# Optimization experiments

Hardware: AMD Instinct MI355X
Metric: run time of the kernel (lower is better)

## Reference

```python
import jax, jax.numpy as jnp
import numpy as np

DIM = 256
N = 8192

def setup_inputs() -> dict:
    key = jax.random.key(0)
    kx, kq, kk, kv = jax.random.split(key, 4)
    X = jax.random.normal(kx, (N, DIM), dtype=jnp.float32)
    # nn.Linear weights are [out, in]; xavier-uniform-like scale via normal/sqrt(dim)
    Wq = jax.random.normal(kq, (DIM, DIM), dtype=jnp.float32) / np.sqrt(DIM)
    Wk = jax.random.normal(kk, (DIM, DIM), dtype=jnp.float32) / np.sqrt(DIM)
    Wv = jax.random.normal(kv, (DIM, DIM), dtype=jnp.float32) / np.sqrt(DIM)
    return {"X": X, "Wq": Wq, "Wk": Wk, "Wv": Wv}

def reference(X, Wq, Wk, Wv):
    # nn.Linear(no bias): y = X @ W.T
    Q = X @ Wq.T  # [N, D]
    K = X @ Wk.T
    V = X @ Wv.T
    scores = (Q @ K.T) / jnp.sqrt(jnp.asarray(DIM, dtype=X.dtype))  # [N, N]
    softed = jax.nn.softmax(scores, axis=-1)
    return softed @ V  # [N, D]
```

## Files before the change

### kernel.cpp

```cpp
#include <hip/hip_runtime.h>
#include <math.h>

#define N 8192
#define D 256
#define QBLK 128
#define KBLK 32

typedef float f32x4 __attribute__((ext_vector_type(4)));
typedef float f32x16 __attribute__((ext_vector_type(16)));
typedef short bf16x8 __attribute__((ext_vector_type(8)));

#define MFMA16(a, b, c) __builtin_amdgcn_mfma_f32_16x16x32_bf16((a), (b), (c), 0, 0, 0)
#define MFMA32(a, b, c) __builtin_amdgcn_mfma_f32_32x32x16_bf16((a), (b), (c), 0, 0, 0)
#define BAR() __builtin_amdgcn_s_barrier()
#define CFENCE() asm volatile("" ::: "memory")

__device__ __forceinline__ unsigned short f2b(float f) {
    unsigned u = __builtin_bit_cast(unsigned, f);
    u = u + 0x7fffu + ((u >> 16) & 1u);
    return (unsigned short)(u >> 16);
}
__device__ __forceinline__ unsigned pk2(float a, float b) {
    return (unsigned)f2b(a) | ((unsigned)f2b(b) << 16);
}
__device__ __forceinline__ unsigned cvtpk(float a, float b) {
    unsigned r;
    asm("v_cvt_pk_bf16_f32 %0, %1, %2" : "=v"(r) : "v"(a), "v"(b));
    return r;
}
__device__ __forceinline__ float b2f(short s) {
    unsigned x = ((unsigned)(unsigned short)s) << 16;
    return __builtin_bit_cast(float, x);
}

__global__ __launch_bounds__(256) void proj_mfma(
    const float* __restrict__ X, const float* __restrict__ Wq,
    const float* __restrict__ Wk, const float* __restrict__ Wv,
    unsigned short* __restrict__ Qb, unsigned short* __restrict__ Kb,
    unsigned short* __restrict__ Vt)
{
    __shared__ char Wl[32768];
    const int z = blockIdx.z;
    const float* W = (z == 0) ? Wq : (z == 1) ? Wk : Wv;
    const int r0 = blockIdx.x * 64;
    const int c0 = blockIdx.y * 64;
    const int t = threadIdx.x, w = t >> 6, l = t & 63;
    const int lo = l & 15, hi = l >> 4;

    #pragma unroll
    for (int i = 0; i < 16; ++i) {
        int e4 = t + i * 256;
        int col = e4 >> 6, kk4 = e4 & 63;
        float4 f = *(const float4*)&W[(size_t)(c0 + col) * D + kk4 * 4];
        unsigned long long v = (unsigned long long)pk2(f.x, f.y)
                             | ((unsigned long long)pk2(f.z, f.w) << 32);
        *(unsigned long long*)(Wl + col * 512 + ((kk4 * 8) ^ ((col & 7) << 4))) = v;
    }
    __syncthreads();

    bf16x8 xf[8];
    {
        const float* xr = X + (size_t)(r0 + w * 16 + lo) * D;
        #pragma unroll
        for (int ks = 0; ks < 8; ++ks) {
            float4 a = *(const float4*)(xr + ks * 32 + hi * 8);
            float4 b = *(const float4*)(xr + ks * 32 + hi * 8 + 4);
            bf16x8 v;
            v[0] = (short)f2b(a.x); v[1] = (short)f2b(a.y);
            v[2] = (short)f2b(a.z); v[3] = (short)f2b(a.w);
            v[4] = (short)f2b(b.x); v[5] = (short)f2b(b.y);
            v[6] = (short)f2b(b.z); v[7] = (short)f2b(b.w);
            xf[ks] = v;
        }
    }

    f32x4 acc[4];
    #pragma unroll
    for (int nc = 0; nc < 4; ++nc) acc[nc] = (f32x4){0.f, 0.f, 0.f, 0.f};
    #pragma unroll
    for (int ks = 0; ks < 8; ++ks) {
        #pragma unroll
        for (int nc = 0; nc < 4; ++nc) {
            int col = nc * 16 + lo;
            bf16x8 wf = *(const bf16x8*)(Wl + col * 512 +
                                         ((ks * 64 + hi * 16) ^ ((col & 7) << 4)));
            acc[nc] = MFMA16(xf[ks], wf, acc[nc]);
        }
    }

    if (z < 2) {
        unsigned short* Y = z ? Kb : Qb;
        #pragma unroll
        for (int nc = 0; nc < 4; ++nc)
            #pragma unroll
            for (int r = 0; r < 4; ++r)
                Y[(size_t)(r0 + w * 16 + hi * 4 + r) * D + c0 + nc * 16 + lo] = f2b(acc[nc][r]);
    } else {
        #pragma unroll
        for (int nc = 0; nc < 4; ++nc) {
            unsigned long long v = (unsigned long long)pk2(acc[nc][0], acc[nc][1])
                                 | ((unsigned long long)pk2(acc[nc][2], acc[nc][3]) << 32);
            *(unsigned long long*)&Vt[(size_t)(c0 + nc * 16 + lo) * N + r0 + w * 16 + hi * 4] = v;
        }
    }
}

template <int KSPLIT>
__global__ __launch_bounds__(256, 2) void attn_mfma(
    const unsigned short* __restrict__ Qb,
    const unsigned short* __restrict__ Kb,
    const unsigned short* __restrict__ Vt,
    unsigned short* __restrict__ Opart,
    float2* __restrict__ ml)
{
    extern __shared__ char smem[];
    const int t = threadIdx.x;
    const int w = t >> 6;
    const int l = t & 63;
    const int r = l & 31;
    const int hi1 = l >> 5;
    const int bid = blockIdx.x;
    const int split = bid % KSPLIT;
    const int xblk = bid / KSPLIT;
    const int q0 = xblk * QBLK + w * 32;
    const int kbase = split * (N / KSPLIT);
    const int NTS = N / KSPLIT / KBLK;
    const int p0 = bid & (NTS - 1);

    unsigned ksoff[4], vsoff[4];
    #pragma unroll
    for (int i = 0; i < 4; ++i) {
        int c = t + i * 256;
        int rr = c >> 5, xc = c & 31;
        int pk = (rr & 0x13) | ((rr & 4) << 1) | ((rr & 8) >> 1);
        ksoff[i] = (unsigned)(pk * D + (xc ^ (rr & 7)) * 8);
        int dd = c >> 2, x2 = c & 3;
        vsoff[i] = (unsigned)(dd * N + (x2 ^ ((dd >> 1) & 3)) * 8);
    }

    auto stageK = [&](char* kbuf, int tile) {
        const unsigned koff = (unsigned)(kbase + tile * KBLK) * D;
        #pragma unroll
        for (int i = 0; i < 4; ++i)
            __builtin_amdgcn_global_load_lds(
                (const __attribute__((address_space(1))) void*)(Kb + koff + ksoff[i]),
                (__attribute__((address_space(3))) void*)(kbuf + (t + i * 256) * 16), 16, 0, 0);
    };
    auto stageV = [&](char* vbuf, int tile) {
        const unsigned voff = (unsigned)(kbase + tile * KBLK);
        #pragma unroll
        for (int i = 0; i < 4; ++i)
            __builtin_amdgcn_global_load_lds(
                (const __attribute__((address_space(1))) void*)(Vt + voff + vsoff[i]),
                (__attribute__((address_space(3))) void*)(vbuf + (t + i * 256) * 16), 16, 0, 0);
    };

    bf16x8 qf[16];
    {
        const unsigned short* qrow = Qb + (size_t)(q0 + r) * D;
        #pragma unroll
        for (int ks = 0; ks < 16; ++ks)
            qf[ks] = *(const bf16x8*)(qrow + ks * 16 + hi1 * 8);
    }

    stageK(smem, p0);
    stageV(smem + 32768, p0);
    stageK(smem + 16384, (p0 + 1) & (NTS - 1));
    stageV(smem + 32768 + 16384, (p0 + 1) & (NTS - 1));

    f32x16 Oacc[8];
    #pragma unroll
    for (int nc = 0; nc < 8; ++nc)
        #pragma unroll
        for (int e = 0; e < 16; ++e) Oacc[nc][e] = 0.f;
    float m_run = -INFINITY, l_run = 0.f;
    const float scale2 = 0.09016994f;

    asm volatile("s_waitcnt vmcnt(8)" ::: "memory");
    BAR();

    for (int tt = 0; tt < NTS; ++tt) {
        const int cur = tt & 1;
        char* Kl = smem + cur * 16384;
        char* Vl = smem + 32768 + cur * 16384;

        f32x16 sacc;
        #pragma unroll
        for (int e = 0; e < 16; ++e) sacc[e] = 0.f;

        bf16x8 kf8[8];
        #pragma unroll
        for (int j = 0; j < 8; ++j)
            kf8[j] = *(const bf16x8*)(Kl + r * 512 + (((j * 2 + hi1) ^ (r & 7)) * 16));
        __builtin_amdgcn_s_setprio(1);
        #pragma unroll
        for (int j = 0; j < 8; ++j)
            sacc = MFMA32(kf8[j], qf[j], sacc);
        __builtin_amdgcn_s_setprio(0);

        bf16x8 kg8[8];
        #pragma unroll
        for (int j = 0; j < 8; ++j)
            kg8[j] = *(const bf16x8*)(Kl + r * 512 + ((((8 + j) * 2 + hi1) ^ (r & 7)) * 16));
        __builtin_amdgcn_s_setprio(1);
        #pragma unroll
        for (int j = 0; j < 8; ++j)
            sacc = MFMA32(kg8[j], qf[8 + j], sacc);
        __builtin_amdgcn_s_setprio(0);

        if (tt + 2 < NTS) {
            CFENCE(); BAR(); CFENCE();
            stageK(Kl, (p0 + tt + 2) & (NTS - 1));
        }

        float m0 = fmaxf(fmaxf(sacc[0], sacc[1]),   fmaxf(sacc[2], sacc[3]));
        float m1 = fmaxf(fmaxf(sacc[4], sacc[5]),   fmaxf(sacc[6], sacc[7]));
        float m2 = fmaxf(fmaxf(sacc[8], sacc[9]),   fmaxf(sacc[10], sacc[11]));
        float m3 = fmaxf(fmaxf(sacc[12], sacc[13]), fmaxf(sacc[14], sacc[15]));
        float pm = fmaxf(fmaxf(m0, m1), fmaxf(m2, m3)) * scale2;

        bool need = pm > m_run + 11.0f;
        if (__builtin_expect(__any(need), 0)) {
            float m2x = fmaxf(pm, __shfl_xor(pm, 32));
            float m_new = fmaxf(m_run, m2x);
            float corr = exp2f(m_run - m_new);
            m_run = m_new;
            l_run *= corr;
            #pragma unroll
            for (int nc = 0; nc < 8; ++nc)
                #pragma unroll
                for (int e = 0; e < 16; ++e) Oacc[nc][e] *= corr;
        }

        bf16x8 pb[2];
        float sum = 0.f;
        #pragma unroll
        for (int s1 = 0; s1 < 2; ++s1) {
            union { unsigned u[4]; bf16x8 v; } uu;
            #pragma unroll
            for (int j2 = 0; j2 < 4; ++j2) {
                float a = __builtin_amdgcn_exp2f(sacc[s1 * 8 + j2 * 2]     * scale2 - m_run);
                float b = __builtin_amdgcn_exp2f(sacc[s1 * 8 + j2 * 2 + 1] * scale2 - m_run);
                sum += a + b;
                uu.u[j2] = cvtpk(a, b);
            }
            pb[s1] = uu.v;
        }
        l_run += sum;

        bf16x8 vf8[8];
        #pragma unroll
        for (int nc = 0; nc < 4; ++nc) {
            const char* vrow = Vl + (nc * 32 + r) * 64;
            vf8[nc * 2 + 0] = *(const bf16x8*)(vrow + (((0 + hi1) ^ ((r >> 1) & 3)) * 16));
            vf8[nc * 2 + 1] = *(const bf16x8*)(vrow + (((2 + hi1) ^ ((r >> 1) & 3)) * 16));
        }
        __builtin_amdgcn_s_setprio(1);
        #pragma unroll
        for (int nc = 0; nc < 4; ++nc) {
            Oacc[nc] = MFMA32(vf8[nc * 2 + 0], pb[0], Oacc[nc]);
            Oacc[nc] = MFMA32(vf8[nc * 2 + 1], pb[1], Oacc[nc]);
        }
        __builtin_amdgcn_s_setprio(0);

        bf16x8 vg8[8];
        #pragma unroll
        for (int nc = 0; nc < 4; ++nc) {
            const char* vrow = Vl + ((nc + 4) * 32 + r) * 64;
            vg8[nc * 2 + 0] = *(const bf16x8*)(vrow + (((0 + hi1) ^ ((r >> 1) & 3)) * 16));
            vg8[nc * 2 + 1] = *(const bf16x8*)(vrow + (((2 + hi1) ^ ((r >> 1) & 3)) * 16));
        }
        __builtin_amdgcn_s_setprio(1);
        #pragma unroll
        for (int nc = 0; nc < 4; ++nc) {
            Oacc[nc + 4] = MFMA32(vg8[nc * 2 + 0], pb[0], Oacc[nc + 4]);
            Oacc[nc + 4] = MFMA32(vg8[nc * 2 + 1], pb[1], Oacc[nc + 4]);
        }
        __builtin_amdgcn_s_setprio(0);

        if (tt + 2 < NTS) {
            CFENCE(); BAR(); CFENCE();
            stageV(Vl, (p0 + tt + 2) & (NTS - 1));
            asm volatile("s_waitcnt vmcnt(8)" ::: "memory");
            BAR(); CFENCE();
        } else if (tt + 1 < NTS) {
            asm volatile("s_waitcnt vmcnt(0)" ::: "memory");
            BAR(); CFENCE();
        }
    }

    l_run += __shfl_xor(l_run, 32);
    const size_t orow = ((size_t)split * N + q0 + r) * D;
    #pragma unroll
    for (int nc = 0; nc < 8; ++nc)
        #pragma unroll
        for (int g = 0; g < 4; ++g) {
            unsigned long long v =
                  (unsigned long long)pk2(Oacc[nc][g * 4 + 0], Oacc[nc][g * 4 + 1])
                | ((unsigned long long)pk2(Oacc[nc][g * 4 + 2], Oacc[nc][g * 4 + 3]) << 32);
            *(unsigned long long*)&Opart[orow + nc * 32 + g * 8 + hi1 * 4] = v;
        }
    if (l < 32)
        ml[(size_t)split * N + q0 + r] = make_float2(m_run, l_run);
}

__global__ __launch_bounds__(256) void combine_kernel(
    const unsigned short* __restrict__ Opart, const float2* __restrict__ ml,
    float* __restrict__ out, int nsplit)
{
    int idx = blockIdx.x * 256 + threadIdx.x;
    int q = idx >> 5;
    int d0 = (idx & 31) * 8;

    float M = -INFINITY;
    for (int i = 0; i < nsplit; ++i) M = fmaxf(M, ml[(size_t)i * N + q].x);
    float L = 0.f;
    float acc[8] = {};
    for (int i = 0; i < nsplit; ++i) {
        float2 v = ml[(size_t)i * N + q];
        float wgt = exp2f(v.x - M);
        L += wgt * v.y;
        bf16x8 ov = *(const bf16x8*)&Opart[((size_t)i * N + q) * D + d0];
        #pragma unroll
        for (int j = 0; j < 8; ++j) acc[j] += wgt * b2f(ov[j]);
    }
    float r = 1.f / L;
    #pragma unroll
    for (int j = 0; j < 8; ++j) out[(size_t)q * D + d0 + j] = acc[j] * r;
}

extern "C" void kernel_launch(void* const* d_in, const int* in_sizes, int n_in,
                              void* d_out, int out_size, void* d_ws, size_t ws_size,
                              hipStream_t stream) {
    const float* X  = (const float*)d_in[0];
    const float* Wq = (const float*)d_in[1];
    const float* Wk = (const float*)d_in[2];
    const float* Wv = (const float*)d_in[3];

    unsigned short* ws = (unsigned short*)d_ws;
    const size_t ndq = (size_t)N * D;
    unsigned short* Qb = ws;
    unsigned short* Kb = ws + ndq;
    unsigned short* Vt = ws + 2 * ndq;
    unsigned short* Opart = ws + 3 * ndq;

    auto need = [ndq](int ks) {
        return (size_t)(3 + ks) * ndq * 2 + (size_t)ks * N * 8;
    };
    const int ksplit = (ws_size >= need(8)) ? 8 : (ws_size >= need(4)) ? 4 : 2;
    float2* ml = (float2*)(ws + (3 + ksplit) * ndq);

    (void)hipFuncSetAttribute((const void*)attn_mfma<8>,
                              hipFuncAttributeMaxDynamicSharedMemorySize, 65536);
    (void)hipFuncSetAttribute((const void*)attn_mfma<4>,
                              hipFuncAttributeMaxDynamicSharedMemorySize, 65536);
    (void)hipFuncSetAttribute((const void*)attn_mfma<2>,
                              hipFuncAttributeMaxDynamicSharedMemorySize, 65536);

    proj_mfma<<<dim3(N / 64, D / 64, 3), 256, 0, stream>>>(X, Wq, Wk, Wv, Qb, Kb, Vt);
    if (ksplit == 8)
        attn_mfma<8><<<dim3((N / QBLK) * 8), 256, 65536, stream>>>(Qb, Kb, Vt, Opart, ml);
    else if (ksplit == 4)
        attn_mfma<4><<<dim3((N / QBLK) * 4), 256, 65536, stream>>>(Qb, Kb, Vt, Opart, ml);
    else
        attn_mfma<2><<<dim3((N / QBLK) * 2), 256, 65536, stream>>>(Qb, Kb, Vt, Opart, ml);
    combine_kernel<<<(N * D / 8) / 256, 256, 0, stream>>>(Opart, ml, (float*)d_out, ksplit);
}
```

Before: 125.6 us.

## Load K and V fragments straight from global memory, dropping LDS staging

Removes the double-buffered LDS staging of K and V tiles, along with its barriers and swizzled offsets. Each wave now loads its MFMA fragments directly from global memory, relying on L1/L2 to serve the reuse across waves. The block grows to 512 threads (8 waves, QBLK 256), halving the grid. This drops LDS traffic and synchronization, but global-load latency is exposed inside the loop with no software prefetch, and the V loads are strided across rows of the transposed V.

```diff
diff --git a/kernel.cpp b/kernel.cpp
--- a/kernel.cpp
+++ b/kernel.cpp
@@ -3,7 +3,7 @@
 
 #define N 8192
 #define D 256
-#define QBLK 128
+#define QBLK 256
 #define KBLK 32
 
 typedef float f32x4 __attribute__((ext_vector_type(4)));
@@ -12,8 +12,6 @@
 
 #define MFMA16(a, b, c) __builtin_amdgcn_mfma_f32_16x16x32_bf16((a), (b), (c), 0, 0, 0)
 #define MFMA32(a, b, c) __builtin_amdgcn_mfma_f32_32x32x16_bf16((a), (b), (c), 0, 0, 0)
-#define BAR() __builtin_amdgcn_s_barrier()
-#define CFENCE() asm volatile("" ::: "memory")
 
 __device__ __forceinline__ unsigned short f2b(float f) {
     unsigned u = __builtin_bit_cast(unsigned, f);
@@ -106,14 +104,13 @@
 }
 
 template <int KSPLIT>
-__global__ __launch_bounds__(256, 2) void attn_mfma(
+__global__ __launch_bounds__(512, 2) void attn_mfma(
     const unsigned short* __restrict__ Qb,
     const unsigned short* __restrict__ Kb,
     const unsigned short* __restrict__ Vt,
     unsigned short* __restrict__ Opart,
     float2* __restrict__ ml)
 {
-    extern __shared__ char smem[];
     const int t = threadIdx.x;
     const int w = t >> 6;
     const int l = t & 63;
@@ -127,33 +124,7 @@
     const int NTS = N / KSPLIT / KBLK;
     const int p0 = bid & (NTS - 1);
 
-    unsigned ksoff[4], vsoff[4];
-    #pragma unroll
-    for (int i = 0; i < 4; ++i) {
-        int c = t + i * 256;
-        int rr = c >> 5, xc = c & 31;
-        int pk = (rr & 0x13) | ((rr & 4) << 1) | ((rr & 8) >> 1);
-        ksoff[i] = (unsigned)(pk * D + (xc ^ (rr & 7)) * 8);
-        int dd = c >> 2, x2 = c & 3;
-        vsoff[i] = (unsigned)(dd * N + (x2 ^ ((dd >> 1) & 3)) * 8);
-    }
-
-    auto stageK = [&](char* kbuf, int tile) {
-        const unsigned koff = (unsigned)(kbase + tile * KBLK) * D;
-        #pragma unroll
-        for (int i = 0; i < 4; ++i)
-            __builtin_amdgcn_global_load_lds(
-                (const __attribute__((address_space(1))) void*)(Kb + koff + ksoff[i]),
-                (__attribute__((address_space(3))) void*)(kbuf + (t + i * 256) * 16), 16, 0, 0);
-    };
-    auto stageV = [&](char* vbuf, int tile) {
-        const unsigned voff = (unsigned)(kbase + tile * KBLK);
-        #pragma unroll
-        for (int i = 0; i < 4; ++i)
-            __builtin_amdgcn_global_load_lds(
-                (const __attribute__((address_space(1))) void*)(Vt + voff + vsoff[i]),
-                (__attribute__((address_space(3))) void*)(vbuf + (t + i * 256) * 16), 16, 0, 0);
-    };
+    const int pk = (r & 0x13) | ((r & 4) << 1) | ((r & 8) >> 1);
 
     bf16x8 qf[16];
     {
@@ -163,10 +134,8 @@
             qf[ks] = *(const bf16x8*)(qrow + ks * 16 + hi1 * 8);
     }
 
-    stageK(smem, p0);
-    stageV(smem + 32768, p0);
-    stageK(smem + 16384, (p0 + 1) & (NTS - 1));
-    stageV(smem + 32768 + 16384, (p0 + 1) & (NTS - 1));
+    const unsigned short* Kp = Kb + (size_t)pk * D + hi1 * 8;
+    const unsigned short* Vp = Vt + (size_t)r * N + hi1 * 8;
 
     f32x16 Oacc[8];
     #pragma unroll
@@ -176,41 +145,38 @@
     float m_run = -INFINITY, l_run = 0.f;
     const float scale2 = 0.09016994f;
 
-    asm volatile("s_waitcnt vmcnt(8)" ::: "memory");
-    BAR();
-
     for (int tt = 0; tt < NTS; ++tt) {
-        const int cur = tt & 1;
-        char* Kl = smem + cur * 16384;
-        char* Vl = smem + 32768 + cur * 16384;
+        const int tile = (p0 + tt) & (NTS - 1);
+        const int kvt = kbase + tile * KBLK;
+
+        const unsigned short* kp = Kp + (size_t)kvt * D;
+        bf16x8 kf8[8], kg8[8];
+        #pragma unroll
+        for (int j = 0; j < 8; ++j) kf8[j] = *(const bf16x8*)(kp + j * 16);
+        #pragma unroll
+        for (int j = 0; j < 8; ++j) kg8[j] = *(const bf16x8*)(kp + 128 + j * 16);
 
         f32x16 sacc;
         #pragma unroll
         for (int e = 0; e < 16; ++e) sacc[e] = 0.f;
-
-        bf16x8 kf8[8];
-        #pragma unroll
-        for (int j = 0; j < 8; ++j)
-            kf8[j] = *(const bf16x8*)(Kl + r * 512 + (((j * 2 + hi1) ^ (r & 7)) * 16));
         __builtin_amdgcn_s_setprio(1);
         #pragma unroll
-        for (int j = 0; j < 8; ++j)
-            sacc = MFMA32(kf8[j], qf[j], sacc);
+        for (int j = 0; j < 8; ++j) sacc = MFMA32(kf8[j], qf[j], sacc);
+        #pragma unroll
+        for (int j = 0; j < 8; ++j) sacc = MFMA32(kg8[j], qf[8 + j], sacc);
         __builtin_amdgcn_s_setprio(0);
 
-        bf16x8 kg8[8];
-        #pragma unroll
-        for (int j = 0; j < 8; ++j)
-            kg8[j] = *(const bf16x8*)(Kl + r * 512 + ((((8 + j) * 2 + hi1) ^ (r & 7)) * 16));
-        __builtin_amdgcn_s_setprio(1);
-        #pragma unroll
-        for (int j = 0; j < 8; ++j)
-            sacc = MFMA32(kg8[j], qf[8 + j], sacc);
-        __builtin_amdgcn_s_setprio(0);
-
-        if (tt + 2 < NTS) {
-            CFENCE(); BAR(); CFENCE();
-            stageK(Kl, (p0 + tt + 2) & (NTS - 1));
+        const unsigned short* vp = Vp + kvt;
+        bf16x8 vf8[8], vg8[8];
+        #pragma unroll
+        for (int nc = 0; nc < 4; ++nc) {
+            vf8[nc * 2 + 0] = *(const bf16x8*)(vp + (size_t)nc * 32 * N);
+            vf8[nc * 2 + 1] = *(const bf16x8*)(vp + (size_t)nc * 32 * N + 16);
+        }
+        #pragma unroll
+        for (int nc = 0; nc < 4; ++nc) {
+            vg8[nc * 2 + 0] = *(const bf16x8*)(vp + (size_t)(nc + 4) * 32 * N);
+            vg8[nc * 2 + 1] = *(const bf16x8*)(vp + (size_t)(nc + 4) * 32 * N + 16);
         }
 
         float m0 = fmaxf(fmaxf(sacc[0], sacc[1]),   fmaxf(sacc[2], sacc[3]));
@@ -248,45 +214,18 @@
         }
         l_run += sum;
 
-        bf16x8 vf8[8];
-        #pragma unroll
-        for (int nc = 0; nc < 4; ++nc) {
-            const char* vrow = Vl + (nc * 32 + r) * 64;
-            vf8[nc * 2 + 0] = *(const bf16x8*)(vrow + (((0 + hi1) ^ ((r >> 1) & 3)) * 16));
-            vf8[nc * 2 + 1] = *(const bf16x8*)(vrow + (((2 + hi1) ^ ((r >> 1) & 3)) * 16));
-        }
         __builtin_amdgcn_s_setprio(1);
         #pragma unroll
         for (int nc = 0; nc < 4; ++nc) {
             Oacc[nc] = MFMA32(vf8[nc * 2 + 0], pb[0], Oacc[nc]);
             Oacc[nc] = MFMA32(vf8[nc * 2 + 1], pb[1], Oacc[nc]);
         }
-        __builtin_amdgcn_s_setprio(0);
-
-        bf16x8 vg8[8];
-        #pragma unroll
-        for (int nc = 0; nc < 4; ++nc) {
-            const char* vrow = Vl + ((nc + 4) * 32 + r) * 64;
-            vg8[nc * 2 + 0] = *(const bf16x8*)(vrow + (((0 + hi1) ^ ((r >> 1) & 3)) * 16));
-            vg8[nc * 2 + 1] = *(const bf16x8*)(vrow + (((2 + hi1) ^ ((r >> 1) & 3)) * 16));
-        }
-        __builtin_amdgcn_s_setprio(1);
         #pragma unroll
         for (int nc = 0; nc < 4; ++nc) {
             Oacc[nc + 4] = MFMA32(vg8[nc * 2 + 0], pb[0], Oacc[nc + 4]);
             Oacc[nc + 4] = MFMA32(vg8[nc * 2 + 1], pb[1], Oacc[nc + 4]);
         }
         __builtin_amdgcn_s_setprio(0);
-
-        if (tt + 2 < NTS) {
-            CFENCE(); BAR(); CFENCE();
-            stageV(Vl, (p0 + tt + 2) & (NTS - 1));
-            asm volatile("s_waitcnt vmcnt(8)" ::: "memory");
-            BAR(); CFENCE();
-        } else if (tt + 1 < NTS) {
-            asm volatile("s_waitcnt vmcnt(0)" ::: "memory");
-            BAR(); CFENCE();
-        }
     }
 
     l_run += __shfl_xor(l_run, 32);
@@ -350,19 +289,12 @@
     const int ksplit = (ws_size >= need(8)) ? 8 : (ws_size >= need(4)) ? 4 : 2;
     float2* ml = (float2*)(ws + (3 + ksplit) * ndq);
 
-    (void)hipFuncSetAttribute((const void*)attn_mfma<8>,
-                              hipFuncAttributeMaxDynamicSharedMemorySize, 65536);
-    (void)hipFuncSetAttribute((const void*)attn_mfma<4>,
-                              hipFuncAttributeMaxDynamicSharedMemorySize, 65536);
-    (void)hipFuncSetAttribute((const void*)attn_mfma<2>,
-                              hipFuncAttributeMaxDynamicSharedMemorySize, 65536);
-
     proj_mfma<<<dim3(N / 64, D / 64, 3), 256, 0, stream>>>(X, Wq, Wk, Wv, Qb, Kb, Vt);
     if (ksplit == 8)
-        attn_mfma<8><<<dim3((N / QBLK) * 8), 256, 65536, stream>>>(Qb, Kb, Vt, Opart, ml);
+        attn_mfma<8><<<dim3((N / QBLK) * 8), 512, 0, stream>>>(Qb, Kb, Vt, Opart, ml);
     else if (ksplit == 4)
-        attn_mfma<4><<<dim3((N / QBLK) * 4), 256, 65536, stream>>>(Qb, Kb, Vt, Opart, ml);
+        attn_mfma<4><<<dim3((N / QBLK) * 4), 512, 0, stream>>>(Qb, Kb, Vt, Opart, ml);
     else
-        attn_mfma<2><<<dim3((N / QBLK) * 2), 256, 65536, stream>>>(Qb, Kb, Vt, Opart, ml);
+        attn_mfma<2><<<dim3((N / QBLK) * 2), 512, 0, stream>>>(Qb, Kb, Vt, Opart, ml);
     combine_kernel<<<(N * D / 8) / 256, 256, 0, stream>>>(Opart, ml, (float*)d_out, ksplit);
 }
```

Result: slower. 335.0 us (+166.8%).
